# Kernel tuning notes

Measured on AMD Instinct MI355X. Metric: run time of the kernel, lower is better.

## Reference

```python
import jax, jax.numpy as jnp
import numpy as np

B, C2D, C3D, H, W, N = 4, 64, 64, 256, 256, 16384
NEG_SLOPE = 0.1


def _conv1x1_lrelu(x, w, b):
    # 1x1 conv (no norm) + leaky_relu(0.1), per Conv2dNormRelu defaults
    y = jnp.einsum('bchw,oc->bohw', x, w) + b[None, :, None, None]
    return jax.nn.leaky_relu(y, NEG_SLOPE)


def _batch_gather(feat, idx):
    # feat: [B, C, N], idx: [B, P] -> [B, C, P]
    return jnp.take_along_axis(feat, idx[:, None, :], axis=2)


def setup_inputs() -> dict:
    key = jax.random.key(0)
    ks = jax.random.split(key, 14)
    f = jax.random.normal
    s = 0.05
    return {
        'xy': jax.random.uniform(ks[0], (B, 2, N), jnp.float32) * jnp.float32(W),
        'feat_2d': f(ks[1], (B, C2D, H, W), jnp.float32),
        'feat_3d': f(ks[2], (B, C3D, N), jnp.float32),
        'last_flow_2d': f(ks[3], (B, 2, H, W), jnp.float32),
        'last_flow_3d_to_2d': f(ks[4], (B, 2, N), jnp.float32),
        'nn_proj': jax.random.randint(ks[5], (B, H, W, 1), 0, N, jnp.int32),
        'w1': f(ks[6], (C3D, C3D + 5), jnp.float32) * s,
        'b1': f(ks[7], (C3D,), jnp.float32) * s,
        'w2': f(ks[8], (C3D, C3D), jnp.float32) * s,
        'b2': f(ks[9], (C3D,), jnp.float32) * s,
        'w3': f(ks[10], (C3D, C3D), jnp.float32) * s,
        'b3': f(ks[11], (C3D,), jnp.float32) * s,
        'wf': f(ks[12], (C2D, C2D + C3D), jnp.float32) * s,
        'bf': f(ks[13], (C2D,), jnp.float32) * s,
    }


def reference(xy, feat_2d, feat_3d, last_flow_2d, last_flow_3d_to_2d, nn_proj,
              w1, b1, w2, b2, w3, b3, wf, bf):
    b, _, h, w = feat_2d.shape
    # concat per-point flow onto 3D features: [B, C3D+2, N]
    feat_3d_aug = jnp.concatenate([feat_3d, last_flow_3d_to_2d], axis=1)

    idx = nn_proj[..., 0].reshape(b, h * w)  # nearest-neighbor point per pixel
    gathered = _batch_gather(feat_3d_aug, idx).reshape(b, -1, h, w)  # [B, C3D+2, H, W]
    xy_proj = _batch_gather(xy, idx).reshape(b, 2, h, w)             # [B, 2, H, W]

    # pixel-coordinate mesh grid: channel 0 = x (width), channel 1 = y (height)
    gy, gx = jnp.meshgrid(jnp.arange(h, dtype=xy.dtype), jnp.arange(w, dtype=xy.dtype), indexing='ij')
    grid = jnp.stack([gx, gy], axis=0)[None]  # [1, 2, H, W]
    offset = xy_proj - grid                    # [B, 2, H, W]

    # correlation between gathered 3D feats and 2D feats (channel mean)
    corr = jnp.mean(gathered[:, :C2D] * feat_2d, axis=1, keepdims=True)  # [B, 1, H, W]

    # last 2 channels are the projected flow; subtract detached last_flow_2d
    flow_ch = gathered[:, -2:] - jax.lax.stop_gradient(last_flow_2d)
    x = jnp.concatenate([corr, offset, gathered[:, :-2], flow_ch], axis=1)  # [B, C3D+5, H, W]

    x = _conv1x1_lrelu(x, w1, b1)
    x = _conv1x1_lrelu(x, w2, b2)
    x = _conv1x1_lrelu(x, w3, b3)
    out = _conv1x1_lrelu(jnp.concatenate([x, feat_2d], axis=1), wf, bf)  # [B, C2D, H, W]
    return out
```

## Files before the change

kernel.cpp:

```cpp
#include <hip/hip_runtime.h>

#define BB 4
#define CH 64
#define HW 65536
#define NN 16384
#define NT 128
#define TW 256
#define XPITCH 72
#define F2PITCH 72
#define W1OFS 0
#define W2OFS 4096
#define W3OFS 8192
#define WFOFS 12288
#define FWS_BYTE 46080
#define PTAB_BYTE 49152
#define PT_ROW 160
#define WS_NEED ((size_t)PTAB_BYTE + (size_t)BB * NN * PT_ROW)

typedef __attribute__((ext_vector_type(8))) short short8;
typedef __attribute__((ext_vector_type(4))) float f32x4;

union frag_u { unsigned short u[8]; short8 v; };
union frag2_u { unsigned short u[8]; unsigned int d[4]; short8 v; };
union row_u  { uint4 q[4]; unsigned short u[32]; };
union half_u { uint4 q[2]; unsigned short u[16]; };

static __device__ __forceinline__ unsigned short f2bf(float x) {
    unsigned int u = __float_as_uint(x);
    return (unsigned short)((u + 0x7fffu + ((u >> 16) & 1u)) >> 16);
}
static __device__ __forceinline__ float bf2f(unsigned short h) {
    return __uint_as_float(((unsigned int)h) << 16);
}
static __device__ __forceinline__ unsigned int cvtpk(float a, float b) {
    unsigned int r;
    asm("v_cvt_pk_bf16_f32 %0, %1, %2" : "=v"(r) : "v"(a), "v"(b));
    return r;
}

__global__ __launch_bounds__(256) void prep(
    const float* __restrict__ xy, const float* __restrict__ f3d,
    const float* __restrict__ lf3d,
    const float* __restrict__ w1, const float* __restrict__ b1,
    const float* __restrict__ w2, const float* __restrict__ b2,
    const float* __restrict__ w3, const float* __restrict__ b3,
    const float* __restrict__ wf, const float* __restrict__ bf,
    unsigned short* __restrict__ wpk, float* __restrict__ fws,
    char* __restrict__ pt)
{
    const int t = threadIdx.x;
    const int bx = blockIdx.x;
    if (bx >= NN / 64) {
        if (blockIdx.y != 0) return;
        const int blk = bx - NN / 64;
        if (blk == 0) {
            for (int i = t; i < 64 * 64; i += 256) {
                const int m = i >> 6, k = i & 63;
                wpk[W1OFS + i] = f2bf(w1[m * 69 + 3 + k]);
            }
        } else if (blk == 1) {
            for (int i = t; i < 64 * 64; i += 256) wpk[W2OFS + i] = f2bf(w2[i]);
        } else if (blk == 2) {
            for (int i = t; i < 64 * 64; i += 256) wpk[W3OFS + i] = f2bf(w3[i]);
        } else if (blk == 3) {
            for (int i = t; i < 64 * 128; i += 256) wpk[WFOFS + i] = f2bf(wf[i]);
        } else if (t < 64) {
            fws[t]       = b1[t];
            fws[64 + t]  = b2[t];
            fws[128 + t] = b3[t];
            fws[192 + t] = bf[t];
            fws[256 + t] = w1[t * 69 + 1];
            fws[320 + t] = w1[t * 69 + 2];
            fws[384 + t] = w1[t * 69 + 0];
            fws[448 + t] = w1[t * 69 + 67];
            fws[512 + t] = w1[t * 69 + 68];
        }
        return;
    }
    const int cq = t >> 6;
    const int l = t & 63;
    const int gn = bx * 64 + l;
    const int b = blockIdx.y;
    half_u r;
#pragma unroll
    for (int i = 0; i < 16; i++)
        r.u[i] = f2bf(f3d[(size_t)(b * CH + cq * 16 + i) * NN + gn]);
    char* row = pt + ((size_t)b * NN + gn) * PT_ROW;
    uint4* rq = (uint4*)row;
    rq[2 * cq] = r.q[0];
    rq[2 * cq + 1] = r.q[1];
    if (cq == 0) {
        float4 e;
        e.x = xy[(size_t)(b * 2 + 0) * NN + gn];
        e.y = xy[(size_t)(b * 2 + 1) * NN + gn];
        e.z = lf3d[(size_t)(b * 2 + 0) * NN + gn];
        e.w = lf3d[(size_t)(b * 2 + 1) * NN + gn];
        *(float4*)(row + 144) = e;
    }
}

static __device__ __forceinline__ void wstage(
    const unsigned short* __restrict__ wpk, unsigned short* wl, int tid)
{
#pragma unroll 1
    for (int m = 0; m < 3; m++) {
        const char* g = (const char*)(wpk + m * 4096);
        char* l = (char*)(wl + m * 4096);
        for (int i = tid; i < 512; i += 256) {
            const int row = i >> 3, cb = (i & 7) * 16;
            const uint4 v = *(const uint4*)(g + row * 128 + cb);
            *(uint4*)(l + row * 128 + (cb ^ ((row & 7) << 4))) = v;
        }
    }
    {
        const char* g = (const char*)(wpk + WFOFS);
        char* l = (char*)(wl + WFOFS);
        for (int i = tid; i < 1024; i += 256) {
            const int row = i >> 4, cb = (i & 15) * 16;
            const uint4 v = *(const uint4*)(g + row * 256 + cb);
            *(uint4*)(l + row * 256 + (cb ^ ((row & 7) << 4))) = v;
        }
    }
}

struct pref_t {
    float4 fv[8];
    row_u g;
    float4 e;
    float lfx, lfy;
};

static __device__ __forceinline__ void tile_load(
    pref_t& P, const float* __restrict__ feat2d, const float* __restrict__ lf2d,
    const char* __restrict__ ptab, int b, int p_base, int w, int lane, int idx)
{
    const int ci = lane >> 3, qd = lane & 7;
    const int px0 = 32 * w + qd * 4;
#pragma unroll
    for (int cc = 0; cc < 8; cc++)
        P.fv[cc] = *(const float4*)(feat2d + (size_t)(b * CH + ci * 8 + cc) * HW + p_base + px0);
    const int cp = lane >> 5, j = lane & 31;
    const int n = 32 * w + j;
    const char* prow = ptab + ((size_t)b * NN + idx) * PT_ROW;
#pragma unroll
    for (int k = 0; k < 4; k++) P.g.q[k] = ((const uint4*)prow)[cp * 4 + k];
    if (cp == 0) {
        P.e = *(const float4*)(prow + 144);
        P.lfx = lf2d[(size_t)(b * 2 + 0) * HW + p_base + n];
        P.lfy = lf2d[(size_t)(b * 2 + 1) * HW + p_base + n];
    }
}

static __device__ __forceinline__ void tile_stage(
    const pref_t& P, unsigned short* F2, unsigned short* Xhi, int w, int lane)
{
    const int ci = lane >> 3, qd = lane & 7;
    const int px0 = 32 * w + qd * 4;
#pragma unroll
    for (int px = 0; px < 4; px++) {
        frag2_u fr;
#pragma unroll
        for (int cc = 0; cc < 4; cc++)
            fr.d[cc] = cvtpk(((const float*)&P.fv[2 * cc])[px], ((const float*)&P.fv[2 * cc + 1])[px]);
        *(short8*)&F2[(px0 + px) * F2PITCH + ci * 8] = fr.v;
    }
    const int cp = lane >> 5, j = lane & 31;
    const int n = 32 * w + j;
    uint4* xp = (uint4*)&Xhi[n * XPITCH + cp * 32];
#pragma unroll
    for (int k = 0; k < 4; k++) xp[k] = P.g.q[k];
}

static __device__ __forceinline__ void tile_corr(
    const pref_t& P, const unsigned short* F2, float* offsS, float* auxS,
    int p_base, int w, int lane)
{
    const int cp = lane >> 5, j = lane & 31;
    const int n = 32 * w + j;
    const int p = p_base + n;
    frag_u f2v[4];
#pragma unroll
    for (int k = 0; k < 4; k++)
        f2v[k].v = *(const short8*)&F2[n * F2PITCH + cp * 32 + k * 8];
    float ca = 0.f;
#pragma unroll
    for (int i = 0; i < 32; i++)
        ca += bf2f(f2v[i >> 3].u[i & 7]) * bf2f(P.g.u[i]);
    ca += __shfl_xor(ca, 32);
    if (cp == 0) {
        offsS[n] = P.e.x - (float)(p & 255);
        offsS[NT + n] = P.e.y - (float)(p >> 8);
        auxS[n] = ca * (1.0f / 64.0f);
        auxS[NT + n] = P.e.z - P.lfx;
        auxS[2 * NT + n] = P.e.w - P.lfy;
    }
}

static __device__ __forceinline__ void layer_l1(
    const unsigned short* wrow, const unsigned short* Xh,
    int w, int ln, int q, int swz, f32x4 acc[4][2])
{
#pragma unroll
    for (int kt = 0; kt < 2; kt++) {
        const int kb = (kt * 32 + q * 8) * 2;
        short8 A[4];
#pragma unroll
        for (int mi = 0; mi < 4; mi++)
            A[mi] = *(const short8*)((const char*)wrow + (mi * 16 + ln) * 128 + (kb ^ swz));
#pragma unroll
        for (int ni = 0; ni < 2; ni++) {
            const int nr = 32 * w + ni * 16 + ln;
            short8 bh = *(const short8*)(Xh + nr * XPITCH + kt * 32 + q * 8);
            __builtin_amdgcn_s_setprio(1);
#pragma unroll
            for (int mi = 0; mi < 4; mi++)
                acc[mi][ni] = __builtin_amdgcn_mfma_f32_16x16x32_bf16(A[mi], bh, acc[mi][ni], 0, 0, 0);
            __builtin_amdgcn_s_setprio(0);
        }
    }
}

template<int RB>
static __device__ __forceinline__ void layer_reg(
    const unsigned short* wrow,
    const unsigned int pkH[4][2][2], const unsigned int pkL[4][2][2],
    int srcA, int srcB, int qh, int ln, int q, int swz, f32x4 acc[4][2])
{
#pragma unroll
    for (int kt = 0; kt < 2; kt++) {
        const int kb = (kt * 32 + q * 8) * 2;
        short8 A[4];
#pragma unroll
        for (int mi = 0; mi < 4; mi++)
            A[mi] = *(const short8*)((const char*)wrow + (mi * 16 + ln) * RB + (kb ^ swz));
#pragma unroll
        for (int ni = 0; ni < 2; ni++) {
            frag2_u bh, bl;
#pragma unroll
            for (int p = 0; p < 4; p++) {
                const int src = (p >> 1) ? srcB : srcA;
                const unsigned h0 = (unsigned)__builtin_amdgcn_ds_bpermute(src, (int)pkH[kt * 2 + 0][ni][p & 1]);
                const unsigned h1 = (unsigned)__builtin_amdgcn_ds_bpermute(src, (int)pkH[kt * 2 + 1][ni][p & 1]);
                bh.d[p] = qh ? h1 : h0;
                const unsigned l0 = (unsigned)__builtin_amdgcn_ds_bpermute(src, (int)pkL[kt * 2 + 0][ni][p & 1]);
                const unsigned l1 = (unsigned)__builtin_amdgcn_ds_bpermute(src, (int)pkL[kt * 2 + 1][ni][p & 1]);
                bl.d[p] = qh ? l1 : l0;
            }
            __builtin_amdgcn_s_setprio(1);
#pragma unroll
            for (int mi = 0; mi < 4; mi++) {
                acc[mi][ni] = __builtin_amdgcn_mfma_f32_16x16x32_bf16(A[mi], bh.v, acc[mi][ni], 0, 0, 0);
                acc[mi][ni] = __builtin_amdgcn_mfma_f32_16x16x32_bf16(A[mi], bl.v, acc[mi][ni], 0, 0, 0);
            }
            __builtin_amdgcn_s_setprio(0);
        }
    }
}

static __device__ __forceinline__ void zero_acc(f32x4 acc[4][2]) {
#pragma unroll
    for (int mi = 0; mi < 4; mi++)
#pragma unroll
        for (int ni = 0; ni < 2; ni++)
#pragma unroll
            for (int r = 0; r < 4; r++) acc[mi][ni][r] = 0.f;
}

static __device__ __forceinline__ void epi_pack(
    f32x4 acc[4][2], const float* __restrict__ fws, int bofs, bool off_fix,
    const float* offsp, const float* auxp,
    unsigned int pkH[4][2][2], unsigned int pkL[4][2][2],
    int w, int ln, int q)
{
#pragma unroll
    for (int mi = 0; mi < 4; mi++) {
        const float4 bias = *(const float4*)(fws + bofs + mi * 16 + q * 4);
        float4 wox = bias, woy = bias, wco = bias, wfx = bias, wfy = bias;
        if (off_fix) {
            wox = *(const float4*)(fws + 256 + mi * 16 + q * 4);
            woy = *(const float4*)(fws + 320 + mi * 16 + q * 4);
            wco = *(const float4*)(fws + 384 + mi * 16 + q * 4);
            wfx = *(const float4*)(fws + 448 + mi * 16 + q * 4);
            wfy = *(const float4*)(fws + 512 + mi * 16 + q * 4);
        }
#pragma unroll
        for (int ni = 0; ni < 2; ni++) {
            const int nr = 32 * w + ni * 16 + ln;
            float ox = 0.f, oy = 0.f, co = 0.f, fx = 0.f, fy = 0.f;
            if (off_fix) {
                ox = offsp[nr]; oy = offsp[NT + nr];
                co = auxp[nr];  fx = auxp[NT + nr]; fy = auxp[2 * NT + nr];
            }
            float av[4];
#pragma unroll
            for (int r = 0; r < 4; r++) {
                float a = acc[mi][ni][r] + ((const float*)&bias)[r];
                if (off_fix) {
                    a += ((const float*)&wox)[r] * ox + ((const float*)&woy)[r] * oy;
                    a += ((const float*)&wco)[r] * co;
                    a += ((const float*)&wfx)[r] * fx + ((const float*)&wfy)[r] * fy;
                }
                av[r] = fmaxf(a, 0.1f * a);
            }
#pragma unroll
            for (int t = 0; t < 2; t++) {
                const unsigned hh = cvtpk(av[2 * t], av[2 * t + 1]);
                const float l0 = av[2 * t]     - __uint_as_float(hh << 16);
                const float l1 = av[2 * t + 1] - __uint_as_float(hh & 0xffff0000u);
                pkH[mi][ni][t] = hh;
                pkL[mi][ni][t] = cvtpk(l0, l1);
            }
        }
    }
}

__global__ __launch_bounds__(256, 2) void fuse(
    const float* __restrict__ feat2d, const float* __restrict__ lf2d,
    const int* __restrict__ nn,
    const unsigned short* __restrict__ wpk, const float* __restrict__ fws,
    const char* __restrict__ ptab,
    float* __restrict__ out)
{
    __shared__ unsigned short Xhi[NT * XPITCH];
    __shared__ unsigned short F2[NT * F2PITCH];
    __shared__ unsigned short Wl[20480];
    __shared__ float offsS[2 * NT];
    __shared__ float auxS[3 * NT];

    const int tid = threadIdx.x;
    const int w = tid >> 6, lane = tid & 63;
    const int q = lane >> 4, ln = lane & 15;
    const int b = blockIdx.y;
    const int p0 = blockIdx.x * TW;
    const int n = 32 * w + (lane & 31);

    const int srcA = (((lane >> 4) & 1) * 32 + ln) * 4;
    const int srcB = srcA + 64;
    const int qh = q >> 1;
    const int swz = (ln & 7) << 4;

    const int idx0 = nn[(size_t)b * HW + p0 + n];
    const int idx1 = nn[(size_t)b * HW + p0 + NT + n];

    pref_t P, Pn;
    tile_load(P, feat2d, lf2d, ptab, b, p0, w, lane, idx0);
    wstage(wpk, Wl, tid);
    __syncthreads();

#pragma unroll 1
    for (int t = 0; t < 2; t++) {
        const int p_base = p0 + t * NT;
        tile_stage(P, F2, Xhi, w, lane);
        if (t == 0)
            tile_load(Pn, feat2d, lf2d, ptab, b, p0 + NT, w, lane, idx1);
        tile_corr(P, F2, offsS, auxS, p_base, w, lane);

        unsigned int pkH[4][2][2], pkL[4][2][2];
        f32x4 acc[4][2];
        zero_acc(acc);
        layer_l1(Wl + W1OFS, Xhi, w, ln, q, swz, acc);
        epi_pack(acc, fws, 0, true, offsS, auxS, pkH, pkL, w, ln, q);
#pragma unroll 1
        for (int l = 0; l < 2; l++) {
            zero_acc(acc);
            layer_reg<128>(Wl + W2OFS + (l << 12), pkH, pkL, srcA, srcB, qh, ln, q, swz, acc);
            epi_pack(acc, fws, 64 + (l << 6), false, offsS, auxS, pkH, pkL, w, ln, q);
        }
        zero_acc(acc);
        layer_reg<256>(Wl + WFOFS, pkH, pkL, srcA, srcB, qh, ln, q, swz, acc);
#pragma unroll
        for (int kt = 2; kt < 4; kt++) {
            const int kb = (kt * 32 + q * 8) * 2;
            short8 A[4];
#pragma unroll
            for (int mi = 0; mi < 4; mi++)
                A[mi] = *(const short8*)((const char*)(Wl + WFOFS) + (mi * 16 + ln) * 256 + (kb ^ swz));
#pragma unroll
            for (int ni = 0; ni < 2; ni++) {
                const int nr = 32 * w + ni * 16 + ln;
                frag_u fh;
                fh.v = *(const short8*)&F2[nr * F2PITCH + (kt - 2) * 32 + q * 8];
                __builtin_amdgcn_s_setprio(1);
#pragma unroll
                for (int mi = 0; mi < 4; mi++)
                    acc[mi][ni] = __builtin_amdgcn_mfma_f32_16x16x32_bf16(A[mi], fh.v, acc[mi][ni], 0, 0, 0);
                __builtin_amdgcn_s_setprio(0);
            }
        }
#pragma unroll
        for (int mi = 0; mi < 4; mi++) {
            const float4 bias = *(const float4*)(fws + 192 + mi * 16 + q * 4);
#pragma unroll
            for (int ni = 0; ni < 2; ni++) {
#pragma unroll
                for (int r = 0; r < 4; r++) {
                    float a = acc[mi][ni][r] + ((const float*)&bias)[r];
                    a = fmaxf(a, 0.1f * a);
                    const int m = mi * 16 + q * 4 + r;
                    out[(size_t)(b * CH + m) * HW + p_base + 32 * w + ni * 16 + ln] = a;
                }
            }
        }
        if (t == 0) P = Pn;
    }
}

__global__ __launch_bounds__(256) void fuse_slow(
    const float* __restrict__ feat2d, const float* __restrict__ lf2d,
    const float* __restrict__ xy, const float* __restrict__ feat3d,
    const float* __restrict__ lf3d, const int* __restrict__ nn,
    const float* __restrict__ w1, const float* __restrict__ b1,
    const float* __restrict__ w2, const float* __restrict__ b2,
    const float* __restrict__ w3, const float* __restrict__ b3,
    const float* __restrict__ wf, const float* __restrict__ bfv,
    float* __restrict__ out)
{
    const int p = blockIdx.x * 256 + threadIdx.x;
    const int b = blockIdx.y;
    const int idx = nn[(size_t)b * HW + p];
    const float* f3 = feat3d + (size_t)b * CH * NN + idx;
    float g[CH];
#pragma unroll
    for (int c = 0; c < CH; c++) g[c] = f3[(size_t)c * NN];
    const float fl3x = lf3d[(size_t)(b * 2 + 0) * NN + idx];
    const float fl3y = lf3d[(size_t)(b * 2 + 1) * NN + idx];
    const float xyx = xy[(size_t)(b * 2 + 0) * NN + idx];
    const float xyy = xy[(size_t)(b * 2 + 1) * NN + idx];
    const float* f2p = feat2d + (size_t)b * CH * HW + p;
    float corr = 0.f;
#pragma unroll
    for (int c = 0; c < CH; c++) corr += f2p[(size_t)c * HW] * g[c];
    corr *= (1.f / 64.f);
    float xin[69];
    xin[0] = corr;
    xin[1] = xyx - (float)(p & 255);
    xin[2] = xyy - (float)(p >> 8);
#pragma unroll
    for (int c = 0; c < CH; c++) xin[3 + c] = g[c];
    xin[67] = fl3x - lf2d[(size_t)(b * 2 + 0) * HW + p];
    xin[68] = fl3y - lf2d[(size_t)(b * 2 + 1) * HW + p];
    float x1[64], x2[64], x3[64], accv[64];
#pragma unroll
    for (int o = 0; o < 64; o++) {
        float a = b1[o];
#pragma unroll
        for (int k = 0; k < 69; k++) a += w1[o * 69 + k] * xin[k];
        x1[o] = (a >= 0.f) ? a : 0.1f * a;
    }
#pragma unroll
    for (int o = 0; o < 64; o++) {
        float a = b2[o];
#pragma unroll
        for (int k = 0; k < 64; k++) a += w2[o * 64 + k] * x1[k];
        x2[o] = (a >= 0.f) ? a : 0.1f * a;
    }
#pragma unroll
    for (int o = 0; o < 64; o++) {
        float a = b3[o];
#pragma unroll
        for (int k = 0; k < 64; k++) a += w3[o * 64 + k] * x2[k];
        x3[o] = (a >= 0.f) ? a : 0.1f * a;
    }
#pragma unroll
    for (int o = 0; o < 64; o++) {
        float a = bfv[o];
#pragma unroll
        for (int k = 0; k < 64; k++) a += wf[o * 128 + k] * x3[k];
        accv[o] = a;
    }
#pragma unroll
    for (int k = 0; k < 64; k++) {
        const float f = f2p[(size_t)k * HW];
#pragma unroll
        for (int o = 0; o < 64; o++) accv[o] += wf[o * 128 + 64 + k] * f;
    }
#pragma unroll
    for (int o = 0; o < 64; o++) {
        float a = accv[o];
        a = (a >= 0.f) ? a : 0.1f * a;
        out[(size_t)(b * CH + o) * HW + p] = a;
    }
}

extern "C" void kernel_launch(void* const* d_in, const int* in_sizes, int n_in,
                              void* d_out, int out_size, void* d_ws, size_t ws_size,
                              hipStream_t stream)
{
    const float* xy   = (const float*)d_in[0];
    const float* f2d  = (const float*)d_in[1];
    const float* f3d  = (const float*)d_in[2];
    const float* lf2d = (const float*)d_in[3];
    const float* lf3d = (const float*)d_in[4];
    const int*   nn   = (const int*)d_in[5];
    const float* w1 = (const float*)d_in[6];
    const float* b1 = (const float*)d_in[7];
    const float* w2 = (const float*)d_in[8];
    const float* b2 = (const float*)d_in[9];
    const float* w3 = (const float*)d_in[10];
    const float* b3 = (const float*)d_in[11];
    const float* wf = (const float*)d_in[12];
    const float* bf = (const float*)d_in[13];

    if (ws_size >= WS_NEED) {
        unsigned short* wpk = (unsigned short*)d_ws;
        float* fws = (float*)((char*)d_ws + FWS_BYTE);
        char* pt = (char*)d_ws + PTAB_BYTE;
        prep<<<dim3(NN / 64 + 5, BB), 256, 0, stream>>>(xy, f3d, lf3d,
                                                        w1, b1, w2, b2, w3, b3, wf, bf,
                                                        wpk, fws, pt);
        fuse<<<dim3(HW / TW, BB), 256, 0, stream>>>(f2d, lf2d, nn, wpk, fws, pt, (float*)d_out);
    } else {
        fuse_slow<<<dim3(HW / 256, BB), 256, 0, stream>>>(f2d, lf2d, xy, f3d, lf3d, nn,
                                                          w1, b1, w2, b2, w3, b3, wf, bf,
                                                          (float*)d_out);
    }
}
```

Measured before the change: 201.4 us.

## Feed gathered point rows directly as MFMA fragments, drop LDS staging and two-tile loop

```diff
diff --git a/kernel.cpp b/kernel.cpp
--- a/kernel.cpp
+++ b/kernel.cpp
@@ -5,13 +5,14 @@
 #define HW 65536
 #define NN 16384
 #define NT 128
-#define TW 256
-#define XPITCH 72
 #define F2PITCH 72
 #define W1OFS 0
 #define W2OFS 4096
 #define W3OFS 8192
 #define WFOFS 12288
+#define W2L 0
+#define W3L 4096
+#define WFL 8192
 #define FWS_BYTE 46080
 #define PTAB_BYTE 49152
 #define PT_ROW 160
@@ -22,7 +23,7 @@
 
 union frag_u { unsigned short u[8]; short8 v; };
 union frag2_u { unsigned short u[8]; unsigned int d[4]; short8 v; };
-union row_u  { uint4 q[4]; unsigned short u[32]; };
+union bfrag { uint4 qv; short8 v; unsigned short u[8]; };
 union half_u { uint4 q[2]; unsigned short u[16]; };
 
 static __device__ __forceinline__ unsigned short f2bf(float x) {
@@ -103,8 +104,8 @@
     const unsigned short* __restrict__ wpk, unsigned short* wl, int tid)
 {
 #pragma unroll 1
-    for (int m = 0; m < 3; m++) {
-        const char* g = (const char*)(wpk + m * 4096);
+    for (int m = 0; m < 2; m++) {
+        const char* g = (const char*)(wpk + W2OFS + m * 4096);
         char* l = (char*)(wl + m * 4096);
         for (int i = tid; i < 512; i += 256) {
             const int row = i >> 3, cb = (i & 7) * 16;
@@ -114,7 +115,7 @@
     }
     {
         const char* g = (const char*)(wpk + WFOFS);
-        char* l = (char*)(wl + WFOFS);
+        char* l = (char*)(wl + WFL);
         for (int i = tid; i < 1024; i += 256) {
             const int row = i >> 4, cb = (i & 15) * 16;
             const uint4 v = *(const uint4*)(g + row * 256 + cb);
@@ -125,34 +126,39 @@
 
 struct pref_t {
     float4 fv[8];
-    row_u g;
+    bfrag g4[2][2];
     float4 e;
     float lfx, lfy;
 };
 
 static __device__ __forceinline__ void tile_load(
     pref_t& P, const float* __restrict__ feat2d, const float* __restrict__ lf2d,
-    const char* __restrict__ ptab, int b, int p_base, int w, int lane, int idx)
+    const char* __restrict__ ptab, int b, int p_base, int w, int lane,
+    int i0, int i1)
 {
     const int ci = lane >> 3, qd = lane & 7;
     const int px0 = 32 * w + qd * 4;
 #pragma unroll
     for (int cc = 0; cc < 8; cc++)
         P.fv[cc] = *(const float4*)(feat2d + (size_t)(b * CH + ci * 8 + cc) * HW + p_base + px0);
-    const int cp = lane >> 5, j = lane & 31;
-    const int n = 32 * w + j;
-    const char* prow = ptab + ((size_t)b * NN + idx) * PT_ROW;
-#pragma unroll
-    for (int k = 0; k < 4; k++) P.g.q[k] = ((const uint4*)prow)[cp * 4 + k];
-    if (cp == 0) {
-        P.e = *(const float4*)(prow + 144);
-        P.lfx = lf2d[(size_t)(b * 2 + 0) * HW + p_base + n];
-        P.lfy = lf2d[(size_t)(b * 2 + 1) * HW + p_base + n];
+    const int q = lane >> 4;
+    const uint4* r0 = (const uint4*)(ptab + ((size_t)b * NN + i0) * PT_ROW);
+    const uint4* r1 = (const uint4*)(ptab + ((size_t)b * NN + i1) * PT_ROW);
+#pragma unroll
+    for (int kt = 0; kt < 2; kt++) {
+        P.g4[0][kt].qv = r0[kt * 4 + (q & 3)];
+        P.g4[1][kt].qv = r1[kt * 4 + (q & 3)];
+    }
+    if (lane < 32) {
+        const char* re = (const char*)(lane >= 16 ? r1 : r0);
+        P.e = *(const float4*)(re + 144);
+        P.lfx = lf2d[(size_t)(b * 2 + 0) * HW + p_base + 32 * w + lane];
+        P.lfy = lf2d[(size_t)(b * 2 + 1) * HW + p_base + 32 * w + lane];
     }
 }
 
 static __device__ __forceinline__ void tile_stage(
-    const pref_t& P, unsigned short* F2, unsigned short* Xhi, int w, int lane)
+    const pref_t& P, unsigned short* F2, int w, int lane)
 {
     const int ci = lane >> 3, qd = lane & 7;
     const int px0 = 32 * w + qd * 4;
@@ -164,59 +170,34 @@
             fr.d[cc] = cvtpk(((const float*)&P.fv[2 * cc])[px], ((const float*)&P.fv[2 * cc + 1])[px]);
         *(short8*)&F2[(px0 + px) * F2PITCH + ci * 8] = fr.v;
     }
-    const int cp = lane >> 5, j = lane & 31;
-    const int n = 32 * w + j;
-    uint4* xp = (uint4*)&Xhi[n * XPITCH + cp * 32];
-#pragma unroll
-    for (int k = 0; k < 4; k++) xp[k] = P.g.q[k];
 }
 
 static __device__ __forceinline__ void tile_corr(
     const pref_t& P, const unsigned short* F2, float* offsS, float* auxS,
-    int p_base, int w, int lane)
-{
-    const int cp = lane >> 5, j = lane & 31;
-    const int n = 32 * w + j;
-    const int p = p_base + n;
-    frag_u f2v[4];
-#pragma unroll
-    for (int k = 0; k < 4; k++)
-        f2v[k].v = *(const short8*)&F2[n * F2PITCH + cp * 32 + k * 8];
-    float ca = 0.f;
-#pragma unroll
-    for (int i = 0; i < 32; i++)
-        ca += bf2f(f2v[i >> 3].u[i & 7]) * bf2f(P.g.u[i]);
-    ca += __shfl_xor(ca, 32);
-    if (cp == 0) {
+    int p_base, int w, int lane, int q, int ln)
+{
+    float ca0 = 0.f, ca1 = 0.f;
+#pragma unroll
+    for (int kt = 0; kt < 2; kt++) {
+        frag_u f0, f1;
+        f0.v = *(const short8*)&F2[(32 * w + ln) * F2PITCH + kt * 32 + q * 8];
+        f1.v = *(const short8*)&F2[(32 * w + 16 + ln) * F2PITCH + kt * 32 + q * 8];
+#pragma unroll
+        for (int j = 0; j < 8; j++) {
+            ca0 += bf2f(f0.u[j]) * bf2f(P.g4[0][kt].u[j]);
+            ca1 += bf2f(f1.u[j]) * bf2f(P.g4[1][kt].u[j]);
+        }
+    }
+    ca0 += __shfl_xor(ca0, 16); ca0 += __shfl_xor(ca0, 32);
+    ca1 += __shfl_xor(ca1, 16); ca1 += __shfl_xor(ca1, 32);
+    if (lane < 32) {
+        const int n = 32 * w + lane;
+        const int p = p_base + n;
         offsS[n] = P.e.x - (float)(p & 255);
         offsS[NT + n] = P.e.y - (float)(p >> 8);
-        auxS[n] = ca * (1.0f / 64.0f);
+        auxS[n] = (lane >= 16 ? ca1 : ca0) * (1.0f / 64.0f);
         auxS[NT + n] = P.e.z - P.lfx;
         auxS[2 * NT + n] = P.e.w - P.lfy;
-    }
-}
-
-static __device__ __forceinline__ void layer_l1(
-    const unsigned short* wrow, const unsigned short* Xh,
-    int w, int ln, int q, int swz, f32x4 acc[4][2])
-{
-#pragma unroll
-    for (int kt = 0; kt < 2; kt++) {
-        const int kb = (kt * 32 + q * 8) * 2;
-        short8 A[4];
-#pragma unroll
-        for (int mi = 0; mi < 4; mi++)
-            A[mi] = *(const short8*)((const char*)wrow + (mi * 16 + ln) * 128 + (kb ^ swz));
-#pragma unroll
-        for (int ni = 0; ni < 2; ni++) {
-            const int nr = 32 * w + ni * 16 + ln;
-            short8 bh = *(const short8*)(Xh + nr * XPITCH + kt * 32 + q * 8);
-            __builtin_amdgcn_s_setprio(1);
-#pragma unroll
-            for (int mi = 0; mi < 4; mi++)
-                acc[mi][ni] = __builtin_amdgcn_mfma_f32_16x16x32_bf16(A[mi], bh, acc[mi][ni], 0, 0, 0);
-            __builtin_amdgcn_s_setprio(0);
-        }
     }
 }
 
@@ -314,16 +295,15 @@
     }
 }
 
-__global__ __launch_bounds__(256, 2) void fuse(
+__global__ __launch_bounds__(256, 3) void fuse(
     const float* __restrict__ feat2d, const float* __restrict__ lf2d,
     const int* __restrict__ nn,
     const unsigned short* __restrict__ wpk, const float* __restrict__ fws,
     const char* __restrict__ ptab,
     float* __restrict__ out)
 {
-    __shared__ unsigned short Xhi[NT * XPITCH];
     __shared__ unsigned short F2[NT * F2PITCH];
-    __shared__ unsigned short Wl[20480];
+    __shared__ unsigned short Wl[16384];
     __shared__ float offsS[2 * NT];
     __shared__ float auxS[3 * NT];
 
@@ -331,77 +311,86 @@
     const int w = tid >> 6, lane = tid & 63;
     const int q = lane >> 4, ln = lane & 15;
     const int b = blockIdx.y;
-    const int p0 = blockIdx.x * TW;
-    const int n = 32 * w + (lane & 31);
+    const int p0 = blockIdx.x * NT;
 
     const int srcA = (((lane >> 4) & 1) * 32 + ln) * 4;
     const int srcB = srcA + 64;
     const int qh = q >> 1;
     const int swz = (ln & 7) << 4;
 
-    const int idx0 = nn[(size_t)b * HW + p0 + n];
-    const int idx1 = nn[(size_t)b * HW + p0 + NT + n];
-
-    pref_t P, Pn;
-    tile_load(P, feat2d, lf2d, ptab, b, p0, w, lane, idx0);
+    const int i0 = nn[(size_t)b * HW + p0 + 32 * w + ln];
+    const int i1 = nn[(size_t)b * HW + p0 + 32 * w + 16 + ln];
+
+    pref_t P;
+    tile_load(P, feat2d, lf2d, ptab, b, p0, w, lane, i0, i1);
     wstage(wpk, Wl, tid);
     __syncthreads();
 
+    short8 A1[2][4];
+#pragma unroll
+    for (int kt = 0; kt < 2; kt++)
+#pragma unroll
+        for (int mi = 0; mi < 4; mi++)
+            A1[kt][mi] = *(const short8*)(wpk + W1OFS + (mi * 16 + ln) * 64 + kt * 32 + q * 8);
+
+    tile_stage(P, F2, w, lane);
+    tile_corr(P, F2, offsS, auxS, p0, w, lane, q, ln);
+
+    unsigned int pkH[4][2][2], pkL[4][2][2];
+    f32x4 acc[4][2];
+    zero_acc(acc);
+#pragma unroll
+    for (int kt = 0; kt < 2; kt++) {
+#pragma unroll
+        for (int ni = 0; ni < 2; ni++) {
+            __builtin_amdgcn_s_setprio(1);
+#pragma unroll
+            for (int mi = 0; mi < 4; mi++)
+                acc[mi][ni] = __builtin_amdgcn_mfma_f32_16x16x32_bf16(A1[kt][mi], P.g4[ni][kt].v, acc[mi][ni], 0, 0, 0);
+            __builtin_amdgcn_s_setprio(0);
+        }
+    }
+    epi_pack(acc, fws, 0, true, offsS, auxS, pkH, pkL, w, ln, q);
 #pragma unroll 1
-    for (int t = 0; t < 2; t++) {
-        const int p_base = p0 + t * NT;
-        tile_stage(P, F2, Xhi, w, lane);
-        if (t == 0)
-            tile_load(Pn, feat2d, lf2d, ptab, b, p0 + NT, w, lane, idx1);
-        tile_corr(P, F2, offsS, auxS, p_base, w, lane);
-
-        unsigned int pkH[4][2][2], pkL[4][2][2];
-        f32x4 acc[4][2];
+    for (int l = 0; l < 2; l++) {
         zero_acc(acc);
-        layer_l1(Wl + W1OFS, Xhi, w, ln, q, swz, acc);
-        epi_pack(acc, fws, 0, true, offsS, auxS, pkH, pkL, w, ln, q);
-#pragma unroll 1
-        for (int l = 0; l < 2; l++) {
-            zero_acc(acc);
-            layer_reg<128>(Wl + W2OFS + (l << 12), pkH, pkL, srcA, srcB, qh, ln, q, swz, acc);
-            epi_pack(acc, fws, 64 + (l << 6), false, offsS, auxS, pkH, pkL, w, ln, q);
-        }
-        zero_acc(acc);
-        layer_reg<256>(Wl + WFOFS, pkH, pkL, srcA, srcB, qh, ln, q, swz, acc);
-#pragma unroll
-        for (int kt = 2; kt < 4; kt++) {
-            const int kb = (kt * 32 + q * 8) * 2;
-            short8 A[4];
+        layer_reg<128>(Wl + W2L + (l << 12), pkH, pkL, srcA, srcB, qh, ln, q, swz, acc);
+        epi_pack(acc, fws, 64 + (l << 6), false, offsS, auxS, pkH, pkL, w, ln, q);
+    }
+    zero_acc(acc);
+    layer_reg<256>(Wl + WFL, pkH, pkL, srcA, srcB, qh, ln, q, swz, acc);
+#pragma unroll
+    for (int kt = 2; kt < 4; kt++) {
+        const int kb = (kt * 32 + q * 8) * 2;
+        short8 A[4];
+#pragma unroll
+        for (int mi = 0; mi < 4; mi++)
+            A[mi] = *(const short8*)((const char*)(Wl + WFL) + (mi * 16 + ln) * 256 + (kb ^ swz));
+#pragma unroll
+        for (int ni = 0; ni < 2; ni++) {
+            const int nr = 32 * w + ni * 16 + ln;
+            frag_u fh;
+            fh.v = *(const short8*)&F2[nr * F2PITCH + (kt - 2) * 32 + q * 8];
+            __builtin_amdgcn_s_setprio(1);
 #pragma unroll
             for (int mi = 0; mi < 4; mi++)
-                A[mi] = *(const short8*)((const char*)(Wl + WFOFS) + (mi * 16 + ln) * 256 + (kb ^ swz));
-#pragma unroll
-            for (int ni = 0; ni < 2; ni++) {
-                const int nr = 32 * w + ni * 16 + ln;
-                frag_u fh;
-                fh.v = *(const short8*)&F2[nr * F2PITCH + (kt - 2) * 32 + q * 8];
-                __builtin_amdgcn_s_setprio(1);
-#pragma unroll
-                for (int mi = 0; mi < 4; mi++)
-                    acc[mi][ni] = __builtin_amdgcn_mfma_f32_16x16x32_bf16(A[mi], fh.v, acc[mi][ni], 0, 0, 0);
-                __builtin_amdgcn_s_setprio(0);
-            }
-        }
-#pragma unroll
-        for (int mi = 0; mi < 4; mi++) {
-            const float4 bias = *(const float4*)(fws + 192 + mi * 16 + q * 4);
-#pragma unroll
-            for (int ni = 0; ni < 2; ni++) {
-#pragma unroll
-                for (int r = 0; r < 4; r++) {
-                    float a = acc[mi][ni][r] + ((const float*)&bias)[r];
-                    a = fmaxf(a, 0.1f * a);
-                    const int m = mi * 16 + q * 4 + r;
-                    out[(size_t)(b * CH + m) * HW + p_base + 32 * w + ni * 16 + ln] = a;
-                }
-            }
-        }
-        if (t == 0) P = Pn;
+                acc[mi][ni] = __builtin_amdgcn_mfma_f32_16x16x32_bf16(A[mi], fh.v, acc[mi][ni], 0, 0, 0);
+            __builtin_amdgcn_s_setprio(0);
+        }
+    }
+#pragma unroll
+    for (int mi = 0; mi < 4; mi++) {
+        const float4 bias = *(const float4*)(fws + 192 + mi * 16 + q * 4);
+#pragma unroll
+        for (int ni = 0; ni < 2; ni++) {
+#pragma unroll
+            for (int r = 0; r < 4; r++) {
+                float a = acc[mi][ni][r] + ((const float*)&bias)[r];
+                a = fmaxf(a, 0.1f * a);
+                const int m = mi * 16 + q * 4 + r;
+                out[(size_t)(b * CH + m) * HW + p0 + 32 * w + ni * 16 + ln] = a;
+            }
+        }
     }
 }
 
@@ -508,7 +497,7 @@
         prep<<<dim3(NN / 64 + 5, BB), 256, 0, stream>>>(xy, f3d, lf3d,
                                                         w1, b1, w2, b2, w3, b3, wf, bf,
                                                         wpk, fws, pt);
-        fuse<<<dim3(HW / TW, BB), 256, 0, stream>>>(f2d, lf2d, nn, wpk, fws, pt, (float*)d_out);
+        fuse<<<dim3(HW / NT, BB), 256, 0, stream>>>(f2d, lf2d, nn, wpk, fws, pt, (float*)d_out);
     } else {
         fuse_slow<<<dim3(HW / 256, BB), 256, 0, stream>>>(f2d, lf2d, xy, f3d, lf3d, nn,
                                                           w1, b1, w2, b2, w3, b3, wf, bf,
```

After: 201.1 us. No clear change (-0.1%).
